# Optimization experiments

Measured on AMD Instinct MI355X. Metric: run time of the kernel, lower is better.

Reference implementation:

```python
import jax, jax.numpy as jnp
import numpy as np
import math

S, H, NH, HD = 2048, 1280, 16, 80
WIN = 64
NW = S // WIN
I = 3420
OUT = 3584
L = 8
FULL_IDX = (3, 7)
MERGE = 4  # spatial_merge_size**2
EPS = 1e-6


def setup_inputs() -> dict:
    key = jax.random.key(0)
    ks = jax.random.split(key, 16)
    w = lambda k, s: jax.random.normal(k, s, jnp.float32) * 0.02
    # rotary tables: half-dim freqs duplicated, as in Qwen2.5-VL vision rotary
    inv_freq = 1.0 / (10000.0 ** (np.arange(0, HD // 2, dtype=np.float32) / (HD // 2)))
    freqs = np.outer(np.arange(S, dtype=np.float32), inv_freq)  # [S, HD/2]
    emb = np.concatenate([freqs, freqs], axis=-1)               # [S, HD]
    return {
        "hidden_states": jax.random.normal(ks[0], (S, H), jnp.float32),
        "full_attn_masks": jnp.ones((1, 1, S, S), jnp.float32),
        "window_attn_masks": jnp.ones((NW, 1, WIN, WIN), jnp.float32),
        "cos": jnp.asarray(np.cos(emb)),
        "sin": jnp.asarray(np.sin(emb)),
        "qkv_w": w(ks[1], (L, 3 * H, H)),
        "qkv_b": w(ks[2], (L, 3 * H)),
        "proj_w": w(ks[3], (L, H, H)),
        "proj_b": w(ks[4], (L, H)),
        "norm1_w": jnp.ones((L, H), jnp.float32),
        "norm2_w": jnp.ones((L, H), jnp.float32),
        "gate_w": w(ks[5], (L, I, H)),
        "gate_b": w(ks[6], (L, I)),
        "up_w": w(ks[7], (L, I, H)),
        "up_b": w(ks[8], (L, I)),
        "down_w": w(ks[9], (L, H, I)),
        "down_b": w(ks[10], (L, H)),
        "ln_q_w": jnp.ones((H,), jnp.float32),
        "m0_w": w(ks[11], (H * MERGE, H * MERGE)),
        "m0_b": w(ks[12], (H * MERGE,)),
        "m2_w": w(ks[13], (OUT, H * MERGE)),
        "m2_b": w(ks[14], (OUT,)),
    }


def rmsnorm(x, w):
    v = jnp.mean(jnp.square(x.astype(jnp.float32)), axis=-1, keepdims=True)
    return (x * jax.lax.rsqrt(v + EPS)) * w


def rotate_half(x):
    x1, x2 = jnp.split(x, 2, axis=-1)
    return jnp.concatenate([-x2, x1], axis=-1)


def apply_rope(q, k, cos, sin):
    return q * cos + rotate_half(q) * sin, k * cos + rotate_half(k) * sin


def attn_full(x, mask, cos, sin, qkv_w, qkv_b, proj_w, proj_b):
    # x: [S, H]; mask: [1, 1, S, S] (additive)
    qkv = (x @ qkv_w.T + qkv_b).reshape(S, 3, NH, HD)
    q, k, v = [t[:, i].transpose(1, 0, 2) for i, t in [(0, qkv), (1, qkv), (2, qkv)]]  # [NH, S, HD]
    q, k = apply_rope(q, k, cos, sin)  # cos/sin [S, HD] broadcast over heads
    aw = jnp.einsum('hsd,htd->hst', q, k) / math.sqrt(HD) + mask[0]
    aw = jax.nn.softmax(aw.astype(jnp.float32), axis=-1)
    o = jnp.einsum('hst,htd->hsd', aw, v).transpose(1, 0, 2).reshape(S, NH * HD)
    return o @ proj_w.T + proj_b


def attn_window(x, mask, cos, sin, qkv_w, qkv_b, proj_w, proj_b):
    xw = x.reshape(NW, WIN, H)
    qkv = (xw @ qkv_w.T + qkv_b).reshape(NW, WIN, 3, NH, HD).transpose(2, 0, 3, 1, 4)
    q, k, v = qkv[0], qkv[1], qkv[2]
    cw = cos.reshape(NW, 1, WIN, HD)
    sw = sin.reshape(NW, 1, WIN, HD)
    q, k = apply_rope(q, k, cw, sw)
    aw = jnp.einsum('whsd,whtd->whst', q, k) / math.sqrt(HD) + mask
    aw = jax.nn.softmax(aw.astype(jnp.float32), axis=-1)
    o = jnp.einsum('whst,whtd->whsd', aw, v).transpose(0, 2, 1, 3).reshape(S, NH * HD)
    return o @ proj_w.T + proj_b


def reference(hidden_states, full_attn_masks, window_attn_masks, cos, sin,
              qkv_w, qkv_b, proj_w, proj_b, norm1_w, norm2_w,
              gate_w, gate_b, up_w, up_b, down_w, down_b,
              ln_q_w, m0_w, m0_b, m2_w, m2_b):
    NEG = jnp.finfo(jnp.float32).min
    fm = (1.0 - full_attn_masks) * NEG
    wm = (1.0 - window_attn_masks) * NEG
    x = hidden_states
    for i in range(L):
        h = rmsnorm(x, norm1_w[i])
        if i in FULL_IDX:
            a = attn_full(h, fm, cos, sin, qkv_w[i], qkv_b[i], proj_w[i], proj_b[i])
        else:
            a = attn_window(h, wm, cos, sin, qkv_w[i], qkv_b[i], proj_w[i], proj_b[i])
        x = x + a
        h = rmsnorm(x, norm2_w[i])
        mlp = (jax.nn.silu(h @ gate_w[i].T + gate_b[i]) * (h @ up_w[i].T + up_b[i])) @ down_w[i].T + down_b[i]
        x = x + mlp
    # patch merger: RMSNorm -> merge 4 tokens -> Linear-GELU-Linear
    h = rmsnorm(x, ln_q_w).reshape(-1, H * MERGE)  # [S/4, 5120]
    h = jax.nn.gelu(h @ m0_w.T + m0_b, approximate=False)
    return h @ m2_w.T + m2_b  # [S/4, OUT]
```

## Files before the change

kernel.cpp:

```cpp
#include <hip/hip_runtime.h>
#include <hip/hip_bf16.h>
#include <math.h>

#define S_LEN 2048
#define HID   1280
#define NHEADS 16
#define HDIM  80
#define HDP   96
#define VROWS 96
#define LAYERS 8
#define IDIM  3420
#define IDIMP 3456
#define MERGED 5120
#define OUTD  3584
#define LWE   19824640LL

typedef __attribute__((ext_vector_type(8))) short short8;
typedef __attribute__((ext_vector_type(4))) float f32x4;
typedef __attribute__((ext_vector_type(16))) float f32x16;
typedef unsigned int u32;
typedef __attribute__((ext_vector_type(4))) u32 u32x4;
typedef __attribute__((address_space(1))) const u32* gptr_t;
typedef __attribute__((address_space(3))) u32* lptr_t;

__device__ inline unsigned short f2b(float f){
  __hip_bfloat16 b = __float2bfloat16(f);
  return __builtin_bit_cast(unsigned short, b);
}
__device__ inline float b2f(unsigned short u){
  return __bfloat162float(__builtin_bit_cast(__hip_bfloat16, u));
}
__device__ inline unsigned pk2(float lo, float hi){
  return (unsigned)f2b(lo) | ((unsigned)f2b(hi) << 16);
}

#define NSEG 42
struct ConvSegs {
  int bpre[NSEG + 1];
  long long srcoff[NSEG];
  long long dstoff[NSEG];
  int srcbase[NSEG];
  int N[NSEG], K[NSEG], Kp[NSEG];
  int rstride[NSEG], roffs[NSEG];
};

__global__ __launch_bounds__(256) void convert_all_kernel(
    ConvSegs cs, int bstart,
    const float* __restrict__ b0, const float* __restrict__ b1,
    const float* __restrict__ b2, const float* __restrict__ b3,
    const float* __restrict__ b4, const float* __restrict__ b5,
    const float* __restrict__ b6,
    unsigned short* __restrict__ dst)
{
  const int b = blockIdx.x + bstart;
  int seg = 0;
  while (seg < NSEG - 1 && cs.bpre[seg + 1] <= b) ++seg;
  const int Kp = cs.Kp[seg], K = cs.K[seg], N = cs.N[seg];
  const int kg = Kp >> 3;
  size_t g = (size_t)(b - cs.bpre[seg]) * 256 + threadIdx.x;
  int k8 = (int)(g % kg);
  int n  = (int)(g / kg);
  int k0 = k8 * 8;
  const float* base;
  switch (cs.srcbase[seg]){
    case 0: base = b0; break; case 1: base = b1; break;
    case 2: base = b2; break; case 3: base = b3; break;
    case 4: base = b4; break; case 5: base = b5; break;
    default: base = b6; break;
  }
  const float* src = base + cs.srcoff[seg];
  u32 out0, out1, out2, out3;
  if (n < N && k0 + 8 <= K){
    const float* s = src + (size_t)n * K + k0;
    f32x4 f0 = __builtin_nontemporal_load((const f32x4*)s);
    f32x4 f1 = __builtin_nontemporal_load((const f32x4*)(s + 4));
    out0 = pk2(f0[0], f0[1]); out1 = pk2(f0[2], f0[3]);
    out2 = pk2(f1[0], f1[1]); out3 = pk2(f1[2], f1[3]);
  } else {
    u32 tmp[4];
    #pragma unroll
    for (int j = 0; j < 4; ++j){
      int ka = k0 + 2 * j;
      float lv = (n < N && ka     < K) ? src[(size_t)n * K + ka]     : 0.f;
      float hv = (n < N && ka + 1 < K) ? src[(size_t)n * K + ka + 1] : 0.f;
      tmp[j] = pk2(lv, hv);
    }
    out0 = tmp[0]; out1 = tmp[1]; out2 = tmp[2]; out3 = tmp[3];
  }
  size_t de = (size_t)cs.dstoff[seg] +
              ((size_t)n * cs.rstride[seg] + cs.roffs[seg]) * Kp + k0;
  u32x4 ov = {out0, out1, out2, out3};
  __builtin_nontemporal_store(ov, (u32x4*)(dst + de));
}

__global__ __launch_bounds__(256) void concat_bias_kernel(
    const float* __restrict__ g, const float* __restrict__ u, float* __restrict__ o)
{
  int L = blockIdx.y;
  int n = blockIdx.x * 256 + threadIdx.x;
  if (n >= 2 * IDIMP) return;
  int c = n >> 1, which = n & 1;
  float v = 0.f;
  if (c < IDIM) v = which ? u[(size_t)L * IDIM + c] : g[(size_t)L * IDIM + c];
  o[(size_t)L * 2 * IDIMP + n] = v;
}

__global__ __launch_bounds__(256) void rmsnorm_kernel(
    const float* __restrict__ x, const float* __restrict__ w,
    unsigned short* __restrict__ out, int H)
{
  int s = blockIdx.x;
  const float* row = x + (size_t)s * H;
  float ss = 0.f;
  for (int c = threadIdx.x; c < H; c += 256){ float v = row[c]; ss += v * v; }
  #pragma unroll
  for (int off = 32; off >= 1; off >>= 1) ss += __shfl_xor(ss, off, 64);
  __shared__ float red[4];
  if ((threadIdx.x & 63) == 0) red[threadIdx.x >> 6] = ss;
  __syncthreads();
  ss = red[0] + red[1] + red[2] + red[3];
  float rs = rsqrtf(ss / H + 1e-6f);
  unsigned short* orow = out + (size_t)s * H;
  for (int c = threadIdx.x; c < H; c += 256) orow[c] = f2b(row[c] * rs * w[c]);
}

template<int EPI, int BM, int BN>
__global__ __launch_bounds__(256) void gemm_kernel(
    const unsigned short* __restrict__ A, int lda,
    const unsigned short* __restrict__ B, int ldb,
    const float* __restrict__ bias, int Nact,
    void* __restrict__ Cv, int ldc,
    const float* __restrict__ res,
    int K)
{
  constexpr int MI = BM / 32;
  constexpr int NI = BN / 32;
  __shared__ __align__(16) unsigned short As[2][BM * 32];
  __shared__ __align__(16) unsigned short Bs[2][BN * 32];
  const int tid  = threadIdx.x;
  const int lane = tid & 63;
  const int wave = tid >> 6;
  const int wm = wave >> 1, wn = wave & 1;
  const int gx = gridDim.x, gy = gridDim.y;
  const int total = gx * gy;
  const int orig = blockIdx.y * gx + blockIdx.x;
  const int q8 = total >> 3, r8 = total & 7;
  const int xcd = orig & 7, loc = orig >> 3;
  const int wg = (xcd < r8 ? xcd * (q8 + 1) : r8 * (q8 + 1) + (xcd - r8) * q8) + loc;
  const int m0 = (wg % gy) * BM, n0 = (wg / gy) * BN;
  const int l16 = lane & 15, lh = lane >> 4;
  const int lrow = lane >> 2;
  const int lcol = lane & 3;
  f32x4 acc[MI][NI] = {};

  auto stage = [&](int bufi, int k0){
    #pragma unroll
    for (int j = 0; j < BM / 64; ++j){
      int chunk = wave * (BM / 64) + j;
      int row  = chunk * 16 + lrow;
      int slot = lcol ^ ((row >> 1) & 3);
      const unsigned short* srcA = A + (size_t)(m0 + row) * lda + k0 + slot * 8;
      __builtin_amdgcn_global_load_lds((gptr_t)srcA, (lptr_t)&As[bufi][chunk * 512], 16, 0, 0);
    }
    #pragma unroll
    for (int j = 0; j < BN / 64; ++j){
      int chunk = wave * (BN / 64) + j;
      int row  = chunk * 16 + lrow;
      int slot = lcol ^ ((row >> 1) & 3);
      const unsigned short* srcB = B + (size_t)(n0 + row) * ldb + k0 + slot * 8;
      __builtin_amdgcn_global_load_lds((gptr_t)srcB, (lptr_t)&Bs[bufi][chunk * 512], 16, 0, 0);
    }
  };

  const int nt = K >> 5;
  stage(0, 0);
  __syncthreads();
  int buf = 0;
  for (int t = 0; t < nt; ++t){
    if (t + 1 < nt) stage(buf ^ 1, (t + 1) << 5);
    short8 af[MI], bfr[NI];
    #pragma unroll
    for (int mi = 0; mi < MI; ++mi){
      int r = wm * (BM / 2) + mi * 16 + l16;
      int sl = lh ^ ((r >> 1) & 3);
      af[mi] = *(const short8*)&As[buf][r * 32 + sl * 8];
    }
    #pragma unroll
    for (int ni = 0; ni < NI; ++ni){
      int r = wn * (BN / 2) + ni * 16 + l16;
      int sl = lh ^ ((r >> 1) & 3);
      bfr[ni] = *(const short8*)&Bs[buf][r * 32 + sl * 8];
    }
    #pragma unroll
    for (int mi = 0; mi < MI; ++mi)
      #pragma unroll
      for (int ni = 0; ni < NI; ++ni)
        acc[mi][ni] = __builtin_amdgcn_mfma_f32_16x16x32_bf16(af[mi], bfr[ni], acc[mi][ni], 0, 0, 0);
    __syncthreads();
    buf ^= 1;
  }

  #pragma unroll
  for (int mi = 0; mi < MI; ++mi){
    int row = m0 + wm * (BM / 2) + mi * 16 + lh * 4;
    #pragma unroll
    for (int ni = 0; ni < NI; ++ni){
      int gn = n0 + wn * (BN / 2) + ni * 16 + l16;
      float bv = (gn < Nact) ? bias[gn] : 0.f;
      #pragma unroll
      for (int r2 = 0; r2 < 4; ++r2){
        float v = acc[mi][ni][r2] + bv;
        if (EPI == 4){
          float partner = __shfl_xor(v, 1);
          if (!(l16 & 1)){
            float r = v / (1.f + __expf(-v)) * partner;
            ((unsigned short*)Cv)[(size_t)(row + r2) * ldc + (gn >> 1)] = f2b(r);
          }
        } else {
          size_t offc = (size_t)(row + r2) * ldc + gn;
          if (EPI == 0)      ((float*)Cv)[offc] = v;
          else if (EPI == 1) ((float*)Cv)[offc] = res[offc] + v;
          else if (EPI == 2) ((unsigned short*)Cv)[offc] = f2b(0.5f * v * (1.0f + erff(v * 0.70710678118f)));
          else               ((unsigned short*)Cv)[offc] = f2b(v);
        }
      }
    }
  }
}

__global__ __launch_bounds__(256) void rope_split_kernel(
    const unsigned short* __restrict__ qkv, const float* __restrict__ cosT,
    const float* __restrict__ sinT,
    unsigned short* __restrict__ qo, unsigned short* __restrict__ ko,
    unsigned short* __restrict__ vt)
{
  __shared__ unsigned short vtile[80][128];
  int id = blockIdx.y * 16 + blockIdx.x;
  int logical = ((id & 7) << 5) + (id >> 3);
  const int h = logical & 15;
  const int s0 = (logical >> 4) * 128;
  const int t = threadIdx.x;
  const int sr = t >> 1, half = t & 1;
  const int s = s0 + sr;
  const unsigned short* row = qkv + (size_t)s * 3840 + h * 80;
  const float* crow = cosT + (size_t)s * 80;
  const float* srow = sinT + (size_t)s * 80;
  const float sgn = half ? 1.f : -1.f;
  #pragma unroll
  for (int g = 0; g < 5; ++g){
    int d  = half * 40 + g * 8;
    int dp = 40 - half * 40 + g * 8;
    short8 q8  = *(const short8*)(row + d);
    short8 k8  = *(const short8*)(row + 1280 + d);
    short8 qp8 = *(const short8*)(row + dp);
    short8 kp8 = *(const short8*)(row + 1280 + dp);
    short8 v8  = *(const short8*)(row + 2560 + d);
    f32x4 c0  = *(const f32x4*)(crow + d);
    f32x4 c1  = *(const f32x4*)(crow + d + 4);
    f32x4 sn0 = *(const f32x4*)(srow + d);
    f32x4 sn1 = *(const f32x4*)(srow + d + 4);
    float cc[8] = {c0[0], c0[1], c0[2], c0[3], c1[0], c1[1], c1[2], c1[3]};
    float ss[8] = {sn0[0], sn0[1], sn0[2], sn0[3], sn1[0], sn1[1], sn1[2], sn1[3]};
    short8 qo8, ko8;
    #pragma unroll
    for (int j = 0; j < 8; ++j){
      float qv = b2f((unsigned short)q8[j]);
      float kv = b2f((unsigned short)k8[j]);
      float qr = sgn * b2f((unsigned short)qp8[j]);
      float kr = sgn * b2f((unsigned short)kp8[j]);
      qo8[j] = (short)f2b(qv * cc[j] + qr * ss[j]);
      ko8[j] = (short)f2b(kv * cc[j] + kr * ss[j]);
      vtile[d + j][sr] = (unsigned short)v8[j];
    }
    size_t qkoff = ((size_t)h * S_LEN + s) * HDP + d;
    *(short8*)(qo + qkoff) = qo8;
    *(short8*)(ko + qkoff) = ko8;
  }
  {
    short8 z = {};
    size_t poff = ((size_t)h * S_LEN + s) * HDP + 80 + half * 8;
    *(short8*)(qo + poff) = z;
    *(short8*)(ko + poff) = z;
  }
  __syncthreads();
  #pragma unroll
  for (int it = 0; it < 5; ++it){
    int j = t + it * 256;
    int d = j >> 4, ch = j & 15;
    u32x4 v = *(const u32x4*)&vtile[d][ch * 8];
    *(u32x4*)(vt + ((size_t)h * VROWS + d) * S_LEN + s0 + ch * 8) = v;
  }
}

#define QKPAD 104
#define VPAD  136
__global__ __launch_bounds__(256) void rope_window_kernel(
    const unsigned short* __restrict__ qkv, const float* __restrict__ cosT,
    const float* __restrict__ sinT, unsigned short* __restrict__ out)
{
  __shared__ __align__(16) unsigned short qs[128][QKPAD];
  __shared__ __align__(16) unsigned short ks[128][QKPAD];
  __shared__ __align__(16) unsigned short vtile[96][VPAD];
  __shared__ unsigned short ot[4][32][88];
  int id = blockIdx.y * 16 + blockIdx.x;
  int logical = ((id & 7) << 5) + (id >> 3);
  const int h = logical & 15;
  const int s0 = (logical >> 4) * 128;
  const int t = threadIdx.x;
  {
    const int sr = t >> 1, half = t & 1;
    const int s = s0 + sr;
    const unsigned short* row = qkv + (size_t)s * 3840 + h * 80;
    const float* crow = cosT + (size_t)s * 80;
    const float* srow = sinT + (size_t)s * 80;
    const float sgn = half ? 1.f : -1.f;
    #pragma unroll
    for (int g = 0; g < 5; ++g){
      int d  = half * 40 + g * 8;
      int dp = 40 - half * 40 + g * 8;
      short8 q8  = *(const short8*)(row + d);
      short8 k8  = *(const short8*)(row + 1280 + d);
      short8 qp8 = *(const short8*)(row + dp);
      short8 kp8 = *(const short8*)(row + 1280 + dp);
      short8 v8  = *(const short8*)(row + 2560 + d);
      f32x4 c0  = *(const f32x4*)(crow + d);
      f32x4 c1  = *(const f32x4*)(crow + d + 4);
      f32x4 sn0 = *(const f32x4*)(srow + d);
      f32x4 sn1 = *(const f32x4*)(srow + d + 4);
      float cc[8] = {c0[0], c0[1], c0[2], c0[3], c1[0], c1[1], c1[2], c1[3]};
      float ss[8] = {sn0[0], sn0[1], sn0[2], sn0[3], sn1[0], sn1[1], sn1[2], sn1[3]};
      short8 qo8, ko8;
      #pragma unroll
      for (int j = 0; j < 8; ++j){
        float qv = b2f((unsigned short)q8[j]);
        float kv = b2f((unsigned short)k8[j]);
        float qr = sgn * b2f((unsigned short)qp8[j]);
        float kr = sgn * b2f((unsigned short)kp8[j]);
        qo8[j] = (short)f2b(qv * cc[j] + qr * ss[j]);
        ko8[j] = (short)f2b(kv * cc[j] + kr * ss[j]);
        vtile[d + j][sr] = (unsigned short)v8[j];
      }
      *(short8*)&qs[sr][d] = qo8;
      *(short8*)&ks[sr][d] = ko8;
    }
    short8 z = {};
    *(short8*)&qs[sr][80 + half * 8] = z;
    *(short8*)&ks[sr][80 + half * 8] = z;
    #pragma unroll
    for (int r9 = 0; r9 < 2; ++r9){
      int task = t + r9 * 256;
      if (task < 16 * 17){
        int rr = task / 17, cc2 = (task % 17) * 8;
        *(short8*)&vtile[80 + rr][cc2] = z;
      }
    }
  }
  __syncthreads();

  const int lane = t & 63;
  const int w = t >> 6;
  const int l31 = lane & 31, lh1 = lane >> 5;
  const int qrl = w * 32;
  const int kv0 = (w >> 1) * 64;

  short8 qa[5];
  #pragma unroll
  for (int kc = 0; kc < 5; ++kc)
    qa[kc] = *(const short8*)&qs[qrl + l31][kc * 16 + lh1 * 8];

  float m_ = -1e30f, l_ = 0.f;
  f32x16 o0 = {}, o1 = {}, o2 = {};
  const float scale = 0.11180339887498949f;

  #pragma unroll
  for (int step = 0; step < 2; ++step){
    int kvl = kv0 + step * 32;
    f32x16 sc = {};
    __builtin_amdgcn_s_setprio(1);
    #pragma unroll
    for (int kc = 0; kc < 5; ++kc){
      short8 kf = *(const short8*)&ks[kvl + l31][kc * 16 + lh1 * 8];
      sc = __builtin_amdgcn_mfma_f32_32x32x16_bf16(kf, qa[kc], sc, 0, 0, 0);
    }
    __builtin_amdgcn_s_setprio(0);
    float tmax = sc[0];
    #pragma unroll
    for (int i = 1; i < 16; ++i) tmax = fmaxf(tmax, sc[i]);
    tmax = fmaxf(tmax, __shfl_xor(tmax, 32)) * scale;
    if (!__all(tmax <= m_ + 8.f)){
      float mnew = fmaxf(m_, tmax);
      float corr = __expf(m_ - mnew);
      l_ *= corr;
      #pragma unroll
      for (int i = 0; i < 16; ++i){ o0[i] *= corr; o1[i] *= corr; o2[i] *= corr; }
      m_ = mnew;
    }
    float p[16];
    float rs = 0.f;
    #pragma unroll
    for (int i = 0; i < 16; ++i){ p[i] = __expf(sc[i] * scale - m_); rs += p[i]; }
    rs += __shfl_xor(rs, 32);
    l_ += rs;
    unsigned wd0[4], wd1[4];
    #pragma unroll
    for (int j = 0; j < 2; ++j){
      unsigned Aj = pk2(p[2 * j],     p[2 * j + 1]);
      unsigned Bj = pk2(p[4 + 2 * j], p[4 + 2 * j + 1]);
      unsigned t0 = __shfl_xor(Aj, 32);
      unsigned t1 = __shfl_xor(Bj, 32);
      wd0[j]     = lh1 ? t1 : Aj;
      wd0[2 + j] = lh1 ? Bj : t0;
      Aj = pk2(p[8 + 2 * j],  p[8 + 2 * j + 1]);
      Bj = pk2(p[12 + 2 * j], p[12 + 2 * j + 1]);
      t0 = __shfl_xor(Aj, 32);
      t1 = __shfl_xor(Bj, 32);
      wd1[j]     = lh1 ? t1 : Aj;
      wd1[2 + j] = lh1 ? Bj : t0;
    }
    __builtin_amdgcn_s_setprio(1);
    #pragma unroll
    for (int kc2 = 0; kc2 < 2; ++kc2){
      u32x4 uw = kc2 ? u32x4{wd1[0], wd1[1], wd1[2], wd1[3]}
                     : u32x4{wd0[0], wd0[1], wd0[2], wd0[3]};
      short8 pb = __builtin_bit_cast(short8, uw);
      int sv = kvl + kc2 * 16 + lh1 * 8;
      o0 = __builtin_amdgcn_mfma_f32_32x32x16_bf16(
          *(const short8*)&vtile[l31][sv],      pb, o0, 0, 0, 0);
      o1 = __builtin_amdgcn_mfma_f32_32x32x16_bf16(
          *(const short8*)&vtile[32 + l31][sv], pb, o1, 0, 0, 0);
      o2 = __builtin_amdgcn_mfma_f32_32x32x16_bf16(
          *(const short8*)&vtile[64 + l31][sv], pb, o2, 0, 0, 0);
    }
    __builtin_amdgcn_s_setprio(0);
  }

  float inv = 1.f / l_;
  #pragma unroll
  for (int r = 0; r < 16; ++r){
    int dl = (r & 3) + 8 * (r >> 2) + 4 * lh1;
    ot[w][l31][dl]      = f2b(o0[r] * inv);
    ot[w][l31][32 + dl] = f2b(o1[r] * inv);
    if (dl < 16) ot[w][l31][64 + dl] = f2b(o2[r] * inv);
  }
  int qq = lane >> 1, half2 = lane & 1;
  #pragma unroll
  for (int j = 0; j < 20; ++j){
    unsigned v = *(const unsigned*)&ot[w][qq][half2 * 40 + j * 2];
    *(unsigned*)&out[(size_t)(s0 + qrl + qq) * HID + h * HDIM + half2 * 40 + j * 2] = v;
  }
}

__global__ __launch_bounds__(256) void flash_full_kernel(
    const unsigned short* __restrict__ q, const unsigned short* __restrict__ k,
    const unsigned short* __restrict__ vt, unsigned short* __restrict__ out)
{
  const int lane = threadIdx.x & 63;
  const int w = threadIdx.x >> 6;
  const int l31 = lane & 31, lh1 = lane >> 5;
  int id = blockIdx.y * gridDim.x + blockIdx.x;
  int logical = ((id & 7) << 7) + (id >> 3);
  const int h = logical >> 6;
  const int qr = (logical & 63) * 32;
  const unsigned short* qh = q + (size_t)h * S_LEN * HDP;
  const unsigned short* kh = k + (size_t)h * S_LEN * HDP;
  const unsigned short* vh = vt + (size_t)h * VROWS * S_LEN;

  short8 qa[5];
  #pragma unroll
  for (int kc = 0; kc < 5; ++kc)
    qa[kc] = *(const short8*)(qh + (size_t)(qr + l31) * HDP + kc * 16 + lh1 * 8);

  float m_ = -1e30f, l_ = 0.f;
  f32x16 o0 = {}, o1 = {}, o2 = {};
  const float scale = 0.11180339887498949f;

  for (int kvt = w * 512; kvt < w * 512 + 512; kvt += 32){
    f32x16 sc = {};
    __builtin_amdgcn_s_setprio(1);
    #pragma unroll
    for (int kc = 0; kc < 5; ++kc){
      short8 kf = *(const short8*)(kh + (size_t)(kvt + l31) * HDP + kc * 16 + lh1 * 8);
      sc = __builtin_amdgcn_mfma_f32_32x32x16_bf16(kf, qa[kc], sc, 0, 0, 0);
    }
    __builtin_amdgcn_s_setprio(0);
    float t = sc[0];
    #pragma unroll
    for (int i = 1; i < 16; ++i) t = fmaxf(t, sc[i]);
    t = fmaxf(t, __shfl_xor(t, 32)) * scale;
    if (!__all(t <= m_ + 8.f)){
      float mnew = fmaxf(m_, t);
      float corr = __expf(m_ - mnew);
      l_ *= corr;
      #pragma unroll
      for (int i = 0; i < 16; ++i){ o0[i] *= corr; o1[i] *= corr; o2[i] *= corr; }
      m_ = mnew;
    }
    float p[16];
    float rs = 0.f;
    #pragma unroll
    for (int i = 0; i < 16; ++i){ p[i] = __expf(sc[i] * scale - m_); rs += p[i]; }
    rs += __shfl_xor(rs, 32);
    l_ += rs;
    unsigned wd0[4], wd1[4];
    #pragma unroll
    for (int j = 0; j < 2; ++j){
      unsigned Aj = pk2(p[2 * j],     p[2 * j + 1]);
      unsigned Bj = pk2(p[4 + 2 * j], p[4 + 2 * j + 1]);
      unsigned t0 = __shfl_xor(Aj, 32);
      unsigned t1 = __shfl_xor(Bj, 32);
      wd0[j]     = lh1 ? t1 : Aj;
      wd0[2 + j] = lh1 ? Bj : t0;
      Aj = pk2(p[8 + 2 * j],  p[8 + 2 * j + 1]);
      Bj = pk2(p[12 + 2 * j], p[12 + 2 * j + 1]);
      t0 = __shfl_xor(Aj, 32);
      t1 = __shfl_xor(Bj, 32);
      wd1[j]     = lh1 ? t1 : Aj;
      wd1[2 + j] = lh1 ? Bj : t0;
    }
    __builtin_amdgcn_s_setprio(1);
    #pragma unroll
    for (int kc2 = 0; kc2 < 2; ++kc2){
      u32x4 uw = kc2 ? u32x4{wd1[0], wd1[1], wd1[2], wd1[3]}
                     : u32x4{wd0[0], wd0[1], wd0[2], wd0[3]};
      short8 pb = __builtin_bit_cast(short8, uw);
      const unsigned short* vb = vh + kvt + kc2 * 16 + lh1 * 8;
      o0 = __builtin_amdgcn_mfma_f32_32x32x16_bf16(
          *(const short8*)(vb + (size_t)(l31)      * S_LEN), pb, o0, 0, 0, 0);
      o1 = __builtin_amdgcn_mfma_f32_32x32x16_bf16(
          *(const short8*)(vb + (size_t)(32 + l31) * S_LEN), pb, o1, 0, 0, 0);
      o2 = __builtin_amdgcn_mfma_f32_32x32x16_bf16(
          *(const short8*)(vb + (size_t)(64 + l31) * S_LEN), pb, o2, 0, 0, 0);
    }
    __builtin_amdgcn_s_setprio(0);
  }

  __shared__ float of[80][33];
  __shared__ float mlsh[4][32][2];
  __shared__ float Lsh[32];
  __shared__ unsigned short ot2[32][88];
  if (lane < 32){ mlsh[w][l31][0] = m_; mlsh[w][l31][1] = l_; }
  __syncthreads();
  float M = fmaxf(fmaxf(mlsh[0][l31][0], mlsh[1][l31][0]),
                  fmaxf(mlsh[2][l31][0], mlsh[3][l31][0]));
  float L = 0.f;
  #pragma unroll
  for (int c = 0; c < 4; ++c) L += __expf(mlsh[c][l31][0] - M) * mlsh[c][l31][1];
  float wgt = __expf(m_ - M);
  if (w == 0 && lane < 32) Lsh[l31] = L;
  #pragma unroll
  for (int rnd = 0; rnd < 4; ++rnd){
    if (w == rnd){
      #pragma unroll
      for (int i = 0; i < 16; ++i){
        int dl = (i & 3) + 8 * (i >> 2) + 4 * lh1;
        if (rnd == 0){
          of[dl][l31]      = wgt * o0[i];
          of[32 + dl][l31] = wgt * o1[i];
          if (dl < 16) of[64 + dl][l31] = wgt * o2[i];
        } else {
          of[dl][l31]      += wgt * o0[i];
          of[32 + dl][l31] += wgt * o1[i];
          if (dl < 16) of[64 + dl][l31] += wgt * o2[i];
        }
      }
    }
    __syncthreads();
  }
  const int tq = threadIdx.x & 31, ds0 = (threadIdx.x >> 5) * 10;
  float Lq = Lsh[tq];
  #pragma unroll
  for (int j = 0; j < 10; ++j)
    ot2[tq][ds0 + j] = f2b(of[ds0 + j][tq] / Lq);
  __syncthreads();
  if (threadIdx.x < 64){
    int qq = threadIdx.x >> 1, half = threadIdx.x & 1;
    #pragma unroll
    for (int j2 = 0; j2 < 20; ++j2){
      unsigned v = *(const unsigned*)&ot2[qq][half * 40 + j2 * 2];
      *(unsigned*)&out[(size_t)(qr + qq) * HID + h * HDIM + half * 40 + j2 * 2] = v;
    }
  }
}

extern "C" void kernel_launch(void* const* d_in, const int* in_sizes, int n_in,
                              void* d_out, int out_size, void* d_ws, size_t ws_size,
                              hipStream_t stream)
{
  const float* hidden = (const float*)d_in[0];
  const float* cosT   = (const float*)d_in[3];
  const float* sinT   = (const float*)d_in[4];
  const float* qkv_w  = (const float*)d_in[5];
  const float* qkv_b  = (const float*)d_in[6];
  const float* proj_w = (const float*)d_in[7];
  const float* proj_b = (const float*)d_in[8];
  const float* norm1_w= (const float*)d_in[9];
  const float* norm2_w= (const float*)d_in[10];
  const float* gate_w = (const float*)d_in[11];
  const float* gate_b = (const float*)d_in[12];
  const float* up_w   = (const float*)d_in[13];
  const float* up_b   = (const float*)d_in[14];
  const float* down_w = (const float*)d_in[15];
  const float* down_b = (const float*)d_in[16];
  const float* ln_q_w = (const float*)d_in[17];
  const float* m0_w   = (const float*)d_in[18];
  const float* m0_b   = (const float*)d_in[19];
  const float* m2_w   = (const float*)d_in[20];
  const float* m2_b   = (const float*)d_in[21];

  char* ws = (char*)d_ws;
  size_t off = 0;
  auto carve = [&](size_t bytes)->char*{
    char* p = ws + off; off += (bytes + 255) & ~(size_t)255; return p;
  };
  float*          x    = (float*)         carve((size_t)S_LEN * HID * 4);
  unsigned short* hbuf = (unsigned short*)carve((size_t)S_LEN * HID * 2);
  unsigned short* qkvb = (unsigned short*)carve((size_t)S_LEN * 3840 * 2);
  unsigned short* qp   = (unsigned short*)carve((size_t)NHEADS * S_LEN * HDP * 2);
  unsigned short* kp   = (unsigned short*)carve((size_t)NHEADS * S_LEN * HDP * 2);
  unsigned short* vtb  = (unsigned short*)carve((size_t)NHEADS * VROWS * S_LEN * 2);
  unsigned short* ao   = (unsigned short*)carve((size_t)S_LEN * HID * 2);
  unsigned short* mlp  = (unsigned short*)carve((size_t)S_LEN * IDIMP * 2);
  unsigned short* mg   = (unsigned short*)carve((size_t)512 * MERGED * 2);
  float*          cbias= (float*)         carve((size_t)LAYERS * 2 * IDIMP * 4);
  unsigned short* wbf  = (unsigned short*)carve((size_t)203161600 * 2);
  (void)ws_size; (void)in_sizes; (void)n_in; (void)out_size;

  ConvSegs cs;
  int totalblocks = 0;
  {
    int si = 0;
    auto add = [&](int base, long long soff, long long doff, int N, int K,
                   int Np, int Kp, int rstride, int roffs){
      cs.bpre[si] = totalblocks;
      cs.srcbase[si] = base; cs.srcoff[si] = soff; cs.dstoff[si] = doff;
      cs.N[si] = N; cs.K[si] = K; cs.Kp[si] = Kp;
      cs.rstride[si] = rstride; cs.roffs[si] = roffs;
      long long groups = (long long)Np * (Kp >> 3);
      totalblocks += (int)((groups + 255) / 256);
      ++si;
    };
    for (long long i = 0; i < LAYERS; ++i){
      add(0, i * 3840LL * HID,        i * LWE + 0,        3840, HID, 3840, HID, 1, 0);
      add(1, i * (long long)HID * HID, i * LWE + 4915200,  HID, HID, HID, HID, 1, 0);
      add(2, i * (long long)IDIM * HID, i * LWE + 6553600,  IDIM, HID, IDIMP, HID, 2, 0);
      add(3, i * (long long)IDIM * HID, i * LWE + 6553600,  IDIM, HID, IDIMP, HID, 2, 1);
      add(4, i * (long long)HID * IDIM, i * LWE + 15400960, HID, IDIM, HID, IDIMP, 1, 0);
    }
    add(5, 0, 8 * LWE,            MERGED, MERGED, MERGED, MERGED, 1, 0);
    add(6, 0, 8 * LWE + 26214400, OUTD,   MERGED, OUTD,   MERGED, 1, 0);
    cs.bpre[NSEG] = totalblocks;
  }

  {
    int chunk = (totalblocks + 3) / 4;
    for (int c = 0; c < 4; ++c){
      int bs = c * chunk;
      int nb = (bs + chunk <= totalblocks) ? chunk : (totalblocks - bs);
      if (nb > 0)
        convert_all_kernel<<<nb, 256, 0, stream>>>(
            cs, bs, qkv_w, proj_w, gate_w, up_w, down_w, m0_w, m2_w, wbf);
    }
  }
  concat_bias_kernel<<<dim3(27, LAYERS), 256, 0, stream>>>(gate_b, up_b, cbias);
  hipMemcpyAsync(x, hidden, (size_t)S_LEN * HID * 4, hipMemcpyDeviceToDevice, stream);

  for (int i = 0; i < LAYERS; ++i){
    unsigned short* wl = wbf + (size_t)i * LWE;
    unsigned short* wqkv = wl;
    unsigned short* wproj= wl + 4915200;
    unsigned short* wgu  = wl + 6553600;
    unsigned short* wdown= wl + 15400960;

    rmsnorm_kernel<<<S_LEN, 256, 0, stream>>>(x, norm1_w + (size_t)i * HID, hbuf, HID);
    gemm_kernel<3,128,128><<<dim3(30, 16), 256, 0, stream>>>(
        hbuf, HID, wqkv, HID, qkv_b + (size_t)i * 3840, 3840,
        qkvb, 3840, nullptr, HID);
    if (i == 3 || i == 7){
      rope_split_kernel<<<dim3(NHEADS, 16), 256, 0, stream>>>(qkvb, cosT, sinT, qp, kp, vtb);
      flash_full_kernel<<<dim3(64, 16), 256, 0, stream>>>(qp, kp, vtb, ao);
    } else {
      rope_window_kernel<<<dim3(16, 16), 256, 0, stream>>>(qkvb, cosT, sinT, ao);
    }
    gemm_kernel<1,64,64><<<dim3(20, 32), 256, 0, stream>>>(
        ao, HID, wproj, HID, proj_b + (size_t)i * HID, HID,
        x, HID, x, HID);
    rmsnorm_kernel<<<S_LEN, 256, 0, stream>>>(x, norm2_w + (size_t)i * HID, hbuf, HID);
    gemm_kernel<4,128,128><<<dim3(54, 16), 256, 0, stream>>>(
        hbuf, HID, wgu, HID, cbias + (size_t)i * 2 * IDIMP, 2 * IDIMP,
        mlp, IDIMP, nullptr, HID);
    gemm_kernel<1,64,64><<<dim3(20, 32), 256, 0, stream>>>(
        mlp, IDIMP, wdown, IDIMP, down_b + (size_t)i * HID, HID,
        x, HID, x, IDIMP);
  }
  unsigned short* wm0 = wbf + 8 * LWE;
  unsigned short* wm2 = wm0 + (size_t)MERGED * MERGED;
  rmsnorm_kernel<<<S_LEN, 256, 0, stream>>>(x, ln_q_w, hbuf, HID);
  gemm_kernel<2,64,64><<<dim3(80, 8), 256, 0, stream>>>(
      hbuf, MERGED, wm0, MERGED, m0_b, MERGED, mg, MERGED, nullptr, MERGED);
  gemm_kernel<0,64,64><<<dim3(56, 8), 256, 0, stream>>>(
      mg, MERGED, wm2, MERGED, m2_b, OUTD, d_out, OUTD, nullptr, MERGED);
}
```

Baseline: 2.406 ms.

## Store residual stream in bf16 and vectorize rmsnorm

The fp32 residual stream x becomes bf16: an initial conversion kernel replaces the memcpy, rmsnorm reads bf16 with 16-byte vector loads, and the residual-add GEMM epilogue reads and writes bf16. This halves residual traffic in rmsnorm and the residual-add epilogues. The window attention kernel also reuses the q shared-memory tile as its output staging buffer, with an added barrier, to cut LDS use. The cost is accuracy: the residual is rounded to bf16 after every add across 8 layers.

```diff
diff --git a/kernel.cpp b/kernel.cpp
--- a/kernel.cpp
+++ b/kernel.cpp
@@ -93,6 +93,16 @@
   __builtin_nontemporal_store(ov, (u32x4*)(dst + de));
 }
 
+__global__ __launch_bounds__(256) void h2b_kernel(
+    const float* __restrict__ in, unsigned short* __restrict__ out)
+{
+  size_t i = ((size_t)blockIdx.x * 256 + threadIdx.x) * 8;
+  f32x4 a = *(const f32x4*)(in + i);
+  f32x4 b = *(const f32x4*)(in + i + 4);
+  u32x4 o = {pk2(a[0], a[1]), pk2(a[2], a[3]), pk2(b[0], b[1]), pk2(b[2], b[3])};
+  *(u32x4*)(out + i) = o;
+}
+
 __global__ __launch_bounds__(256) void concat_bias_kernel(
     const float* __restrict__ g, const float* __restrict__ u, float* __restrict__ o)
 {
@@ -106,13 +116,20 @@
 }
 
 __global__ __launch_bounds__(256) void rmsnorm_kernel(
-    const float* __restrict__ x, const float* __restrict__ w,
+    const unsigned short* __restrict__ x, const float* __restrict__ w,
     unsigned short* __restrict__ out, int H)
 {
   int s = blockIdx.x;
-  const float* row = x + (size_t)s * H;
+  const unsigned short* row = x + (size_t)s * H;
+  const int c8 = threadIdx.x;
+  const bool act = c8 < (H >> 3);
+  float vals[8];
   float ss = 0.f;
-  for (int c = threadIdx.x; c < H; c += 256){ float v = row[c]; ss += v * v; }
+  if (act){
+    short8 v8 = *(const short8*)(row + c8 * 8);
+    #pragma unroll
+    for (int j = 0; j < 8; ++j){ vals[j] = b2f((unsigned short)v8[j]); ss += vals[j] * vals[j]; }
+  }
   #pragma unroll
   for (int off = 32; off >= 1; off >>= 1) ss += __shfl_xor(ss, off, 64);
   __shared__ float red[4];
@@ -120,8 +137,15 @@
   __syncthreads();
   ss = red[0] + red[1] + red[2] + red[3];
   float rs = rsqrtf(ss / H + 1e-6f);
-  unsigned short* orow = out + (size_t)s * H;
-  for (int c = threadIdx.x; c < H; c += 256) orow[c] = f2b(row[c] * rs * w[c]);
+  if (act){
+    f32x4 w0 = *(const f32x4*)(w + c8 * 8);
+    f32x4 w1 = *(const f32x4*)(w + c8 * 8 + 4);
+    u32x4 o = {pk2(vals[0] * rs * w0[0], vals[1] * rs * w0[1]),
+               pk2(vals[2] * rs * w0[2], vals[3] * rs * w0[3]),
+               pk2(vals[4] * rs * w1[0], vals[5] * rs * w1[1]),
+               pk2(vals[6] * rs * w1[2], vals[7] * rs * w1[3])};
+    *(u32x4*)(out + (size_t)s * H + c8 * 8) = o;
+  }
 }
 
 template<int EPI, int BM, int BN>
@@ -130,7 +154,7 @@
     const unsigned short* __restrict__ B, int ldb,
     const float* __restrict__ bias, int Nact,
     void* __restrict__ Cv, int ldc,
-    const float* __restrict__ res,
+    const void* __restrict__ res,
     int K)
 {
   constexpr int MI = BM / 32;
@@ -219,7 +243,8 @@
         } else {
           size_t offc = (size_t)(row + r2) * ldc + gn;
           if (EPI == 0)      ((float*)Cv)[offc] = v;
-          else if (EPI == 1) ((float*)Cv)[offc] = res[offc] + v;
+          else if (EPI == 1) ((unsigned short*)Cv)[offc] =
+                                f2b(v + b2f(((const unsigned short*)res)[offc]));
           else if (EPI == 2) ((unsigned short*)Cv)[offc] = f2b(0.5f * v * (1.0f + erff(v * 0.70710678118f)));
           else               ((unsigned short*)Cv)[offc] = f2b(v);
         }
@@ -301,7 +326,7 @@
   __shared__ __align__(16) unsigned short qs[128][QKPAD];
   __shared__ __align__(16) unsigned short ks[128][QKPAD];
   __shared__ __align__(16) unsigned short vtile[96][VPAD];
-  __shared__ unsigned short ot[4][32][88];
+  unsigned short (*ot)[32][88] = (unsigned short(*)[32][88])&qs[0][0];
   int id = blockIdx.y * 16 + blockIdx.x;
   int logical = ((id & 7) << 5) + (id >> 3);
   const int h = logical & 15;
@@ -367,6 +392,7 @@
   #pragma unroll
   for (int kc = 0; kc < 5; ++kc)
     qa[kc] = *(const short8*)&qs[qrl + l31][kc * 16 + lh1 * 8];
+  __syncthreads();
 
   float m_ = -1e30f, l_ = 0.f;
   f32x16 o0 = {}, o1 = {}, o2 = {};
@@ -612,7 +638,7 @@
   auto carve = [&](size_t bytes)->char*{
     char* p = ws + off; off += (bytes + 255) & ~(size_t)255; return p;
   };
-  float*          x    = (float*)         carve((size_t)S_LEN * HID * 4);
+  unsigned short* x    = (unsigned short*)carve((size_t)S_LEN * HID * 2);
   unsigned short* hbuf = (unsigned short*)carve((size_t)S_LEN * HID * 2);
   unsigned short* qkvb = (unsigned short*)carve((size_t)S_LEN * 3840 * 2);
   unsigned short* qp   = (unsigned short*)carve((size_t)NHEADS * S_LEN * HDP * 2);
@@ -662,7 +688,7 @@
     }
   }
   concat_bias_kernel<<<dim3(27, LAYERS), 256, 0, stream>>>(gate_b, up_b, cbias);
-  hipMemcpyAsync(x, hidden, (size_t)S_LEN * HID * 4, hipMemcpyDeviceToDevice, stream);
+  h2b_kernel<<<(int)((size_t)S_LEN * HID / 8 / 256), 256, 0, stream>>>(hidden, x);
 
   for (int i = 0; i < LAYERS; ++i){
     unsigned short* wl = wbf + (size_t)i * LWE;
```

New measurement: 2.357 ms. 1.02x faster.
